# Performance work log

Hardware: AMD Instinct MI355X
Metric: run time of the kernel (lower is better)

The kernel has to match this reference:

```python
import jax, jax.numpy as jnp
import numpy as np

N, E, D, H, G, C = 50000, 800000, 3, 128, 64, 10

def setup_inputs() -> dict:
    key = jax.random.key(0)
    ks = jax.random.split(key, 10)
    s = 0.1  # small init scale
    return {
        "pos": jax.random.normal(ks[0], (N, D), jnp.float32),
        "edge_index": jax.random.randint(ks[1], (2, E), 0, N, dtype=jnp.int64),
        "batch": jnp.sort(jax.random.randint(ks[2], (N,), 0, G, dtype=jnp.int64)),
        "W1": jax.random.normal(ks[3], (D, H), jnp.float32) * s,
        "b1": jnp.zeros((H,), jnp.float32),
        "W2": jax.random.normal(ks[4], (H, H), jnp.float32) * s,
        "b2": jnp.zeros((H,), jnp.float32),
        "W3": jax.random.normal(ks[5], (H, H), jnp.float32) * s,
        "b3": jnp.zeros((H,), jnp.float32),
        "Wl1": jax.random.normal(ks[6], (H, H // 2), jnp.float32) * s,
        "bl1": jnp.zeros((H // 2,), jnp.float32),
        "Wl2": jax.random.normal(ks[7], (H // 2, C), jnp.float32) * s,
        "bl2": jnp.zeros((C,), jnp.float32),
        "num_graphs": G,
    }

def reference(pos, edge_index, batch, W1, b1, W2, b2, W3, b3, Wl1, bl1, Wl2, bl2, num_graphs):
    n = pos.shape[0]
    loop = jnp.arange(n, dtype=edge_index.dtype)
    # GCN: add self-loops, symmetric normalization deg^-1/2 (A+I) deg^-1/2
    src = jnp.concatenate([edge_index[0], loop])
    dst = jnp.concatenate([edge_index[1], loop])
    deg = jax.ops.segment_sum(jnp.ones(src.shape, pos.dtype), dst, num_segments=n)
    dinv = jax.lax.rsqrt(jnp.maximum(deg, 1e-12))  # deg >= 1 due to self-loops
    norm = dinv[src] * dinv[dst]  # [E+N]

    def gcn(x, W, b):
        h = x @ W                               # [N,F] dense transform first (PyG order)
        msg = h[src] * norm[:, None]            # gather + normalize
        return jax.ops.segment_sum(msg, dst, num_segments=n) + b  # scatter-add

    x = jax.nn.relu(gcn(pos, W1, b1))   # dropout = identity (eval mode)
    x = jax.nn.relu(gcn(x, W2, b2))
    x = jax.nn.relu(gcn(x, W3, b3))
    # global_mean_pool over batch ids
    sums = jax.ops.segment_sum(x, batch, num_segments=num_graphs)
    cnt = jax.ops.segment_sum(jnp.ones((n,), x.dtype), batch, num_segments=num_graphs)
    g = sums / jnp.maximum(cnt, 1.0)[:, None]   # [G,H]
    h = jax.nn.relu(g @ Wl1 + bl1)
    return h @ Wl2 + bl2
```

## Files before the change

kernel.cpp:

```cpp
#include <hip/hip_runtime.h>

#define H 128
#define CAP 64
#define LSTRIDE 136
#define PSTR 132
typedef unsigned int uint32;
typedef unsigned short ushort16;
typedef __attribute__((ext_vector_type(8))) short bf16x8;
typedef __attribute__((ext_vector_type(4))) float f32x4;

static __device__ __forceinline__ ushort16 f2bf(float f){
  uint32 u = __float_as_uint(f);
  uint32 r = (u + 0x7fff + ((u >> 16) & 1)) >> 16;
  return (ushort16)r;
}
static __device__ __forceinline__ float bflo(uint32 u){ return __uint_as_float(u << 16); }
static __device__ __forceinline__ float bfhi(uint32 u){ return __uint_as_float(u & 0xffff0000u); }

__global__ __launch_bounds__(256) void k_setup(int* __restrict__ deg, float* __restrict__ gsum,
                                               const int* __restrict__ batch, int n, int G,
                                               int* __restrict__ gb, int SB,
                                               const float* __restrict__ W2, const float* __restrict__ W3,
                                               ushort16* __restrict__ wp2, ushort16* __restrict__ wp3,
                                               float4* __restrict__ y0,
                                               unsigned short* __restrict__ ybA,
                                               unsigned short* __restrict__ ybB){
  int b = blockIdx.x;
  if (b < SB){
    int i = b*256 + threadIdx.x;
    if (i < n) deg[i] = 0;
    if (i < G*H) gsum[i] = 0.f;
    if (i < H){ ybA[(size_t)n*H + i] = 0; ybB[(size_t)n*H + i] = 0; }
    if (i == 0) y0[n] = make_float4(0.f, 0.f, 0.f, 0.f);
    if (i <= G){
      int lo = 0, hi = n;
      while (lo < hi){ int m = (lo + hi) >> 1; if (batch[m] < i) lo = m + 1; else hi = m; }
      gb[i] = lo;
    }
  } else {
    int gid = (b - SB)*256 + threadIdx.x;
    const float* W = (gid < 2048) ? W2 : W3;
    ushort16* wp   = (gid < 2048) ? wp2 : wp3;
    int tid = gid & 2047;
    int frag = tid >> 6, lane = tid & 63;
    int kt = frag >> 3, ct = frag & 7;
    int m = lane & 15, quad = lane >> 4;
    const float* wrow = &W[(kt*32 + quad*8)*H + ct*16 + m];
    ushort16 vals[8];
    #pragma unroll
    for (int j = 0; j < 8; j++) vals[j] = f2bf(wrow[j*H]);
    uint4 o;
    o.x = (uint32)vals[0] | ((uint32)vals[1] << 16);
    o.y = (uint32)vals[2] | ((uint32)vals[3] << 16);
    o.z = (uint32)vals[4] | ((uint32)vals[5] << 16);
    o.w = (uint32)vals[6] | ((uint32)vals[7] << 16);
    *(uint4*)&wp[(size_t)tid*8] = o;
  }
}

__global__ __launch_bounds__(256) void k_count(const int* __restrict__ dst, int E,
                                               int* __restrict__ deg, unsigned short* __restrict__ rank){
  int i = blockIdx.x*256 + threadIdx.x;
  if (i < E) rank[i] = (unsigned short)atomicAdd(&deg[dst[i]], 1);
}

__global__ __launch_bounds__(256) void k_scatter(const int* __restrict__ src, const int* __restrict__ dst,
                                                 int E, int SCB, const unsigned short* __restrict__ rank,
                                                 unsigned short* __restrict__ csr_src,
                                                 const int* __restrict__ deg, const float* __restrict__ pos,
                                                 float4* __restrict__ y0, int n){
  int b = blockIdx.x;
  if (b < SCB){
    int i = b*256 + threadIdx.x;
    if (i < E){
      int r = rank[i];
      if (r < CAP) csr_src[((size_t)dst[i] << 6) + r] = (unsigned short)src[i];
    }
  } else {
    int i = (b - SCB)*256 + threadIdx.x;
    if (i < n){
      float dv = rsqrtf((float)(deg[i] + 1));
      y0[i] = make_float4(pos[3*i]*dv, pos[3*i+1]*dv, pos[3*i+2]*dv, 0.f);
    }
  }
}

__global__ __launch_bounds__(256) void k_layer1(const float4* __restrict__ y0, const int* __restrict__ deg,
      const unsigned short* __restrict__ csr_src,
      const float* __restrict__ W1, const float* __restrict__ b1,
      ushort16* __restrict__ y1, int n){
  int node = blockIdx.x*256 + threadIdx.x;
  if (node >= n) return;
  int cnt = deg[node];
  int lo = node << 6;
  float4 own = y0[node];
  float x = own.x, y = own.y, z = own.z;
  int mm = cnt > CAP ? CAP : cnt;
  int nfull = mm >> 3, rem = mm & 7;
  #define GADD(s0,s1,s2,s3,s4,s5,s6,s7) { \
    float4 v0 = y0[s0], v1 = y0[s1], v2 = y0[s2], v3 = y0[s3]; \
    float4 v4 = y0[s4], v5 = y0[s5], v6 = y0[s6], v7 = y0[s7]; \
    x += ((v0.x+v1.x)+(v2.x+v3.x)) + ((v4.x+v5.x)+(v6.x+v7.x)); \
    y += ((v0.y+v1.y)+(v2.y+v3.y)) + ((v4.y+v5.y)+(v6.y+v7.y)); \
    z += ((v0.z+v1.z)+(v2.z+v3.z)) + ((v4.z+v5.z)+(v6.z+v7.z)); }
  if (rem){
    uint4 iv = *(const uint4*)&csr_src[lo + nfull*8];
    int s0 = (int)(iv.x & 0xffff);
    int s1 = (1 < rem)? (int)(iv.x >> 16)    : n;
    int s2 = (2 < rem)? (int)(iv.y & 0xffff) : n;
    int s3 = (3 < rem)? (int)(iv.y >> 16)    : n;
    int s4 = (4 < rem)? (int)(iv.z & 0xffff) : n;
    int s5 = (5 < rem)? (int)(iv.z >> 16)    : n;
    int s6 = (6 < rem)? (int)(iv.w & 0xffff) : n;
    int s7 = (7 < rem)? (int)(iv.w >> 16)    : n;
    GADD(s0,s1,s2,s3,s4,s5,s6,s7);
  }
  if (nfull){
    uint4 iv = *(const uint4*)&csr_src[lo];
    for (int c = 0; c < nfull; c++){
      uint4 nx = *(const uint4*)&csr_src[lo + c*8 + 8];
      int s0 = iv.x & 0xffff, s1 = iv.x >> 16;
      int s2 = iv.y & 0xffff, s3 = iv.y >> 16;
      int s4 = iv.z & 0xffff, s5 = iv.z >> 16;
      int s6 = iv.w & 0xffff, s7 = iv.w >> 16;
      GADD(s0,s1,s2,s3,s4,s5,s6,s7);
      iv = nx;
    }
  }
  #undef GADD
  float dn = rsqrtf((float)(cnt + 1));
  x *= dn; y *= dn; z *= dn;
  ushort16* rowp = &y1[(size_t)node*H];
  for (int c8 = 0; c8 < 16; c8++){
    float4 wa0 = *(const float4*)&W1[c8*8];
    float4 wa1 = *(const float4*)&W1[c8*8+4];
    float4 wb0 = *(const float4*)&W1[H + c8*8];
    float4 wb1 = *(const float4*)&W1[H + c8*8+4];
    float4 wc0 = *(const float4*)&W1[2*H + c8*8];
    float4 wc1 = *(const float4*)&W1[2*H + c8*8+4];
    float4 bb0 = *(const float4*)&b1[c8*8];
    float4 bb1 = *(const float4*)&b1[c8*8+4];
    float o0 = fmaxf(x*wa0.x + y*wb0.x + z*wc0.x + bb0.x, 0.f) * dn;
    float o1 = fmaxf(x*wa0.y + y*wb0.y + z*wc0.y + bb0.y, 0.f) * dn;
    float o2 = fmaxf(x*wa0.z + y*wb0.z + z*wc0.z + bb0.z, 0.f) * dn;
    float o3 = fmaxf(x*wa0.w + y*wb0.w + z*wc0.w + bb0.w, 0.f) * dn;
    float o4 = fmaxf(x*wa1.x + y*wb1.x + z*wc1.x + bb1.x, 0.f) * dn;
    float o5 = fmaxf(x*wa1.y + y*wb1.y + z*wc1.y + bb1.y, 0.f) * dn;
    float o6 = fmaxf(x*wa1.z + y*wb1.z + z*wc1.z + bb1.z, 0.f) * dn;
    float o7 = fmaxf(x*wa1.w + y*wb1.w + z*wc1.w + bb1.w, 0.f) * dn;
    uint4 o;
    o.x = (uint32)f2bf(o0) | ((uint32)f2bf(o1) << 16);
    o.y = (uint32)f2bf(o2) | ((uint32)f2bf(o3) << 16);
    o.z = (uint32)f2bf(o4) | ((uint32)f2bf(o5) << 16);
    o.w = (uint32)f2bf(o6) | ((uint32)f2bf(o7) << 16);
    *(uint4*)&rowp[c8*8] = o;
  }
}

template<int POOL>
__global__ __launch_bounds__(256) void k_aggdense(const ushort16* __restrict__ y, const int* __restrict__ deg,
      const unsigned short* __restrict__ csr_src, const ushort16* __restrict__ wp,
      const float* __restrict__ bias,
      ushort16* __restrict__ yout, const int* __restrict__ batch, float* __restrict__ gsum, int n){
  __shared__ unsigned short As[16*LSTRIDE];
  __shared__ float pool[POOL ? 16*PSTR : 1];
  __shared__ unsigned short outs[POOL ? 1 : 16*PSTR];
  __shared__ int sbatch[POOL ? 16 : 1];
  __shared__ float sdinv[POOL ? 1 : 16];
  int tid = threadIdx.x;
  int node16 = blockIdx.x*16;
  int nl = tid >> 4;
  int node = node16 + nl;
  int f8 = (tid & 15) * 8;

  if (tid < 16){
    int nn = node16 + tid;
    if (POOL) sbatch[tid] = (nn < n) ? batch[nn] : -1;
    else      sdinv[tid]  = (nn < n) ? rsqrtf((float)(deg[nn] + 1)) : 0.f;
  }

  float a0=0,a1=0,a2=0,a3=0,a4=0,a5=0,a6=0,a7=0;
  float dn = 0.f;
  #define ADDU(u) { a0+=bflo(u.x); a1+=bfhi(u.x); a2+=bflo(u.y); a3+=bfhi(u.y); \
                    a4+=bflo(u.z); a5+=bfhi(u.z); a6+=bflo(u.w); a7+=bfhi(u.w); }
  #define GATHER8(s0,s1,s2,s3,s4,s5,s6,s7) { \
    uint4 u0 = *(const uint4*)&y[(size_t)(s0)*H + f8]; \
    uint4 u1 = *(const uint4*)&y[(size_t)(s1)*H + f8]; \
    uint4 u2 = *(const uint4*)&y[(size_t)(s2)*H + f8]; \
    uint4 u3 = *(const uint4*)&y[(size_t)(s3)*H + f8]; \
    uint4 u4 = *(const uint4*)&y[(size_t)(s4)*H + f8]; \
    uint4 u5 = *(const uint4*)&y[(size_t)(s5)*H + f8]; \
    uint4 u6 = *(const uint4*)&y[(size_t)(s6)*H + f8]; \
    uint4 u7 = *(const uint4*)&y[(size_t)(s7)*H + f8]; \
    ADDU(u0); ADDU(u1); ADDU(u2); ADDU(u3); \
    ADDU(u4); ADDU(u5); ADDU(u6); ADDU(u7); }
  if (node < n){
    int cnt = deg[node];
    int lo = node << 6;
    dn = rsqrtf((float)(cnt + 1));
    uint4 uo = *(const uint4*)&y[(size_t)node*H + f8];
    ADDU(uo);
    int mm = cnt > CAP ? CAP : cnt;
    int nfull = mm >> 3, rem = mm & 7;
    if (rem){
      uint4 iv = *(const uint4*)&csr_src[lo + nfull*8];
      int s0 = (int)(iv.x & 0xffff);
      int s1 = (1 < rem)? (int)(iv.x >> 16)    : n;
      int s2 = (2 < rem)? (int)(iv.y & 0xffff) : n;
      int s3 = (3 < rem)? (int)(iv.y >> 16)    : n;
      int s4 = (4 < rem)? (int)(iv.z & 0xffff) : n;
      int s5 = (5 < rem)? (int)(iv.z >> 16)    : n;
      int s6 = (6 < rem)? (int)(iv.w & 0xffff) : n;
      int s7 = (7 < rem)? (int)(iv.w >> 16)    : n;
      GATHER8(s0,s1,s2,s3,s4,s5,s6,s7);
    }
    if (nfull){
      uint4 iv = *(const uint4*)&csr_src[lo];
      for (int c = 0; c < nfull; c++){
        uint4 nx = *(const uint4*)&csr_src[lo + c*8 + 8];
        int s0 = iv.x & 0xffff, s1 = iv.x >> 16;
        int s2 = iv.y & 0xffff, s3 = iv.y >> 16;
        int s4 = iv.z & 0xffff, s5 = iv.z >> 16;
        int s6 = iv.w & 0xffff, s7 = iv.w >> 16;
        GATHER8(s0,s1,s2,s3,s4,s5,s6,s7);
        iv = nx;
      }
    }
  }
  #undef GATHER8
  #undef ADDU
  uint4 o;
  o.x = (uint32)f2bf(a0*dn) | ((uint32)f2bf(a1*dn) << 16);
  o.y = (uint32)f2bf(a2*dn) | ((uint32)f2bf(a3*dn) << 16);
  o.z = (uint32)f2bf(a4*dn) | ((uint32)f2bf(a5*dn) << 16);
  o.w = (uint32)f2bf(a6*dn) | ((uint32)f2bf(a7*dn) << 16);
  *(uint4*)&As[nl*LSTRIDE + f8] = o;
  __syncthreads();

  int wave = tid >> 6;
  int lane = tid & 63;
  int m = lane & 15, quad = lane >> 4;
  f32x4 acc0 = {0.f,0.f,0.f,0.f}, acc1 = {0.f,0.f,0.f,0.f};
  int ct0 = wave*2, ct1 = wave*2 + 1;
  #pragma unroll
  for (int kt = 0; kt < 4; kt++){
    bf16x8 af = *(const bf16x8*)&As[m*LSTRIDE + kt*32 + quad*8];
    bf16x8 b0 = *(const bf16x8*)&wp[(size_t)((kt*8+ct0)*64 + lane)*8];
    bf16x8 b1 = *(const bf16x8*)&wp[(size_t)((kt*8+ct1)*64 + lane)*8];
    acc0 = __builtin_amdgcn_mfma_f32_16x16x32_bf16(af, b0, acc0, 0, 0, 0);
    acc1 = __builtin_amdgcn_mfma_f32_16x16x32_bf16(af, b1, acc1, 0, 0, 0);
  }
  #pragma unroll
  for (int j = 0; j < 2; j++){
    int ct = wave*2 + j;
    int col = ct*16 + m;
    float bv = bias[col];
    f32x4 ac = j ? acc1 : acc0;
    #pragma unroll
    for (int r = 0; r < 4; r++){
      int rl = quad*4 + r;
      int orow = node16 + rl;
      if (orow < n){
        float v = fmaxf(ac[r] + bv, 0.f);
        if (POOL) pool[rl*PSTR + col] = v;
        else      outs[rl*PSTR + col] = f2bf(v * sdinv[rl]);
      }
    }
  }
  __syncthreads();
  if (POOL){
    int col = tid & 127;
    int half = tid >> 7;
    float run = 0.f; int gprev = -1;
    for (int r = half*8; r < half*8 + 8; r++){
      int g = sbatch[r];
      if (g < 0) break;
      if (g != gprev){
        if (gprev >= 0) atomicAdd(&gsum[gprev*H + col], run);
        run = 0.f; gprev = g;
      }
      run += pool[r*PSTR + col];
    }
    if (gprev >= 0) atomicAdd(&gsum[gprev*H + col], run);
  } else {
    int row = tid >> 4;
    int orow = node16 + row;
    if (orow < n){
      const unsigned short* sp = &outs[row*PSTR + f8];
      uint4 v;
      v.x = (uint32)sp[0] | ((uint32)sp[1] << 16);
      v.y = (uint32)sp[2] | ((uint32)sp[3] << 16);
      v.z = (uint32)sp[4] | ((uint32)sp[5] << 16);
      v.w = (uint32)sp[6] | ((uint32)sp[7] << 16);
      *(uint4*)&yout[(size_t)orow*H + f8] = v;
    }
  }
}

__global__ __launch_bounds__(64) void k_head(const float* __restrict__ gsum, const int* __restrict__ gb,
            const float* __restrict__ Wl1, const float* __restrict__ bl1,
            const float* __restrict__ Wl2, const float* __restrict__ bl2,
            float* __restrict__ out){
  int g = blockIdx.x;
  int t = threadIdx.x;
  __shared__ float gs[H];
  __shared__ float h1[64];
  float inv = 1.f / fmaxf((float)(gb[g+1] - gb[g]), 1.f);
  gs[t]      = gsum[g*H + t]      * inv;
  gs[64 + t] = gsum[g*H + 64 + t] * inv;
  __syncthreads();
  float acc = bl1[t];
  for (int k = 0; k < H; k++) acc += gs[k] * Wl1[k*64 + t];
  h1[t] = fmaxf(acc, 0.f);
  __syncthreads();
  if (t < 10){
    float o = bl2[t];
    for (int j = 0; j < 64; j++) o += h1[j] * Wl2[j*10 + t];
    out[g*10 + t] = o;
  }
}

extern "C" void kernel_launch(void* const* d_in, const int* in_sizes, int n_in,
                              void* d_out, int out_size, void* d_ws, size_t ws_size,
                              hipStream_t stream){
  const float* pos = (const float*)d_in[0];
  const int*  ei   = (const int*)d_in[1];
  const int*  batch= (const int*)d_in[2];
  const float* W1 = (const float*)d_in[3];
  const float* b1 = (const float*)d_in[4];
  const float* W2 = (const float*)d_in[5];
  const float* b2 = (const float*)d_in[6];
  const float* W3 = (const float*)d_in[7];
  const float* b3 = (const float*)d_in[8];
  const float* Wl1 = (const float*)d_in[9];
  const float* bl1 = (const float*)d_in[10];
  const float* Wl2 = (const float*)d_in[11];
  const float* bl2 = (const float*)d_in[12];
  float* out = (float*)d_out;

  int N = in_sizes[0] / 3;
  int E = in_sizes[1] / 2;
  int G = out_size / 10;
  int SB = (N + 255) / 256;
  int SCB = (E + 255) / 256;
  int PB = (N + 255) / 256;

  char* p = (char*)d_ws;
  auto carve = [&](size_t bytes)->char* { char* q = p; p += (bytes + 255) & ~(size_t)255; return q; };
  int*            deg     = (int*)     carve(sizeof(int)    * (size_t)N);
  int*            gb      = (int*)     carve(sizeof(int)    * (size_t)(G+1));
  float*          gsum    = (float*)   carve(sizeof(float)  * (size_t)G * H);
  unsigned short* csr_src = (unsigned short*)carve(sizeof(unsigned short) * (size_t)(N+1) * CAP);
  unsigned short* rank    = (unsigned short*)carve(sizeof(unsigned short) * (size_t)E);
  float4*         y0      = (float4*)  carve(sizeof(float4) * (size_t)(N+1));
  ushort16*       ybufA   = (ushort16*)carve(sizeof(ushort16) * (size_t)(N+1) * H);
  ushort16*       ybufB   = (ushort16*)carve(sizeof(ushort16) * (size_t)(N+1) * H);
  ushort16*       wp2     = (ushort16*)carve(sizeof(ushort16) * 16384);
  ushort16*       wp3     = (ushort16*)carve(sizeof(ushort16) * 16384);

  const int* src = ei;
  const int* dst = ei + E;

  hipLaunchKernelGGL(k_setup, dim3(SB + 16), dim3(256), 0, stream,
                     deg, gsum, batch, N, G, gb, SB, W2, W3, wp2, wp3,
                     y0, (unsigned short*)ybufA, (unsigned short*)ybufB);

  hipLaunchKernelGGL(k_count, dim3((E+255)/256), dim3(256), 0, stream, dst, E, deg, rank);

  hipLaunchKernelGGL(k_scatter, dim3(SCB + PB), dim3(256), 0, stream,
                     src, dst, E, SCB, rank, csr_src, deg, pos, y0, N);

  hipLaunchKernelGGL(k_layer1, dim3((N+255)/256), dim3(256), 0, stream, y0, deg, csr_src, W1, b1, ybufA, N);

  hipLaunchKernelGGL(k_aggdense<0>, dim3((N+15)/16), dim3(256), 0, stream,
                     ybufA, deg, csr_src, wp2, b2, ybufB, (const int*)nullptr, (float*)nullptr, N);

  hipLaunchKernelGGL(k_aggdense<1>, dim3((N+15)/16), dim3(256), 0, stream,
                     ybufB, deg, csr_src, wp3, b3, (ushort16*)nullptr, batch, gsum, N);

  hipLaunchKernelGGL(k_head, dim3(G), dim3(64), 0, stream, gsum, gb, Wl1, bl1, Wl2, bl2, out);
}
```

Before: 230.8 us.

## Split feature buffers into column planes and separate aggregation from dense MFMA

```diff
diff --git a/kernel.cpp b/kernel.cpp
--- a/kernel.cpp
+++ b/kernel.cpp
@@ -16,6 +16,7 @@
 }
 static __device__ __forceinline__ float bflo(uint32 u){ return __uint_as_float(u << 16); }
 static __device__ __forceinline__ float bfhi(uint32 u){ return __uint_as_float(u & 0xffff0000u); }
+
 
 __global__ __launch_bounds__(256) void k_setup(int* __restrict__ deg, float* __restrict__ gsum,
                                                const int* __restrict__ batch, int n, int G,
@@ -28,9 +29,13 @@
   int b = blockIdx.x;
   if (b < SB){
     int i = b*256 + threadIdx.x;
+    size_t PL = (size_t)(n+1)*32;
     if (i < n) deg[i] = 0;
     if (i < G*H) gsum[i] = 0.f;
-    if (i < H){ ybA[(size_t)n*H + i] = 0; ybB[(size_t)n*H + i] = 0; }
+    if (i < H){
+      size_t a = (size_t)(i>>5)*PL + (size_t)n*32 + (i&31);
+      ybA[a] = 0; ybB[a] = 0;
+    }
     if (i == 0) y0[n] = make_float4(0.f, 0.f, 0.f, 0.f);
     if (i <= G){
       int lo = 0, hi = n;
@@ -88,9 +93,10 @@
 __global__ __launch_bounds__(256) void k_layer1(const float4* __restrict__ y0, const int* __restrict__ deg,
       const unsigned short* __restrict__ csr_src,
       const float* __restrict__ W1, const float* __restrict__ b1,
-      ushort16* __restrict__ y1, int n){
+      unsigned short* __restrict__ y1, int n){
   int node = blockIdx.x*256 + threadIdx.x;
   if (node >= n) return;
+  size_t PL = (size_t)(n+1)*32;
   int cnt = deg[node];
   int lo = node << 6;
   float4 own = y0[node];
@@ -130,7 +136,6 @@
   #undef GADD
   float dn = rsqrtf((float)(cnt + 1));
   x *= dn; y *= dn; z *= dn;
-  ushort16* rowp = &y1[(size_t)node*H];
   for (int c8 = 0; c8 < 16; c8++){
     float4 wa0 = *(const float4*)&W1[c8*8];
     float4 wa1 = *(const float4*)&W1[c8*8+4];
@@ -153,15 +158,81 @@
     o.y = (uint32)f2bf(o2) | ((uint32)f2bf(o3) << 16);
     o.z = (uint32)f2bf(o4) | ((uint32)f2bf(o5) << 16);
     o.w = (uint32)f2bf(o6) | ((uint32)f2bf(o7) << 16);
-    *(uint4*)&rowp[c8*8] = o;
-  }
+    *(uint4*)&y1[(size_t)(c8>>2)*PL + (size_t)node*32 + (c8&3)*8] = o;
+  }
+}
+
+__global__ __launch_bounds__(128) void k_aggcol(const unsigned short* __restrict__ y,
+      const int* __restrict__ deg, const unsigned short* __restrict__ csr_src,
+      unsigned short* __restrict__ agg, int n){
+  int b = blockIdx.x;
+  int c = b & 7;
+  int plane = c >> 1;
+  int node16 = ((b >> 3)*2 + (c & 1)) * 16;
+  int tid = threadIdx.x;
+  int nl = tid >> 3;
+  int node = node16 + nl;
+  if (node >= n) return;
+  int l4 = (tid & 7) * 4;
+  size_t PL = (size_t)(n+1)*32;
+  const unsigned short* yp = y + (size_t)plane*PL + l4;
+
+  float a0=0,a1=0,a2=0,a3=0;
+  #define ADDU2(u) { a0+=bflo(u.x); a1+=bfhi(u.x); a2+=bflo(u.y); a3+=bfhi(u.y); }
+  #define GATH8(s0,s1,s2,s3,s4,s5,s6,s7) { \
+    uint2 u0 = *(const uint2*)&yp[(size_t)(s0)*32]; \
+    uint2 u1 = *(const uint2*)&yp[(size_t)(s1)*32]; \
+    uint2 u2 = *(const uint2*)&yp[(size_t)(s2)*32]; \
+    uint2 u3 = *(const uint2*)&yp[(size_t)(s3)*32]; \
+    uint2 u4 = *(const uint2*)&yp[(size_t)(s4)*32]; \
+    uint2 u5 = *(const uint2*)&yp[(size_t)(s5)*32]; \
+    uint2 u6 = *(const uint2*)&yp[(size_t)(s6)*32]; \
+    uint2 u7 = *(const uint2*)&yp[(size_t)(s7)*32]; \
+    ADDU2(u0); ADDU2(u1); ADDU2(u2); ADDU2(u3); \
+    ADDU2(u4); ADDU2(u5); ADDU2(u6); ADDU2(u7); }
+  int cnt = deg[node];
+  int lo = node << 6;
+  uint2 uo = *(const uint2*)&yp[(size_t)node*32];
+  ADDU2(uo);
+  int mm = cnt > CAP ? CAP : cnt;
+  int nfull = mm >> 3, rem = mm & 7;
+  if (rem){
+    uint4 iv = *(const uint4*)&csr_src[lo + nfull*8];
+    int s0 = (int)(iv.x & 0xffff);
+    int s1 = (1 < rem)? (int)(iv.x >> 16)    : n;
+    int s2 = (2 < rem)? (int)(iv.y & 0xffff) : n;
+    int s3 = (3 < rem)? (int)(iv.y >> 16)    : n;
+    int s4 = (4 < rem)? (int)(iv.z & 0xffff) : n;
+    int s5 = (5 < rem)? (int)(iv.z >> 16)    : n;
+    int s6 = (6 < rem)? (int)(iv.w & 0xffff) : n;
+    int s7 = (7 < rem)? (int)(iv.w >> 16)    : n;
+    GATH8(s0,s1,s2,s3,s4,s5,s6,s7);
+  }
+  if (nfull){
+    uint4 iv = *(const uint4*)&csr_src[lo];
+    for (int cc = 0; cc < nfull; cc++){
+      uint4 nx = *(const uint4*)&csr_src[lo + cc*8 + 8];
+      int s0 = iv.x & 0xffff, s1 = iv.x >> 16;
+      int s2 = iv.y & 0xffff, s3 = iv.y >> 16;
+      int s4 = iv.z & 0xffff, s5 = iv.z >> 16;
+      int s6 = iv.w & 0xffff, s7 = iv.w >> 16;
+      GATH8(s0,s1,s2,s3,s4,s5,s6,s7);
+      iv = nx;
+    }
+  }
+  #undef GATH8
+  #undef ADDU2
+  float dn = rsqrtf((float)(cnt + 1));
+  uint2 o;
+  o.x = (uint32)f2bf(a0*dn) | ((uint32)f2bf(a1*dn) << 16);
+  o.y = (uint32)f2bf(a2*dn) | ((uint32)f2bf(a3*dn) << 16);
+  *(uint2*)&agg[(size_t)plane*PL + (size_t)node*32 + l4] = o;
 }
 
 template<int POOL>
-__global__ __launch_bounds__(256) void k_aggdense(const ushort16* __restrict__ y, const int* __restrict__ deg,
-      const unsigned short* __restrict__ csr_src, const ushort16* __restrict__ wp,
-      const float* __restrict__ bias,
-      ushort16* __restrict__ yout, const int* __restrict__ batch, float* __restrict__ gsum, int n){
+__global__ __launch_bounds__(256) void k_dense(const unsigned short* __restrict__ agg,
+      const int* __restrict__ deg, const ushort16* __restrict__ wp, const float* __restrict__ bias,
+      unsigned short* __restrict__ yout, const int* __restrict__ batch, float* __restrict__ gsum, int n){
   __shared__ unsigned short As[16*LSTRIDE];
   __shared__ float pool[POOL ? 16*PSTR : 1];
   __shared__ unsigned short outs[POOL ? 1 : 16*PSTR];
@@ -172,69 +243,16 @@
   int nl = tid >> 4;
   int node = node16 + nl;
   int f8 = (tid & 15) * 8;
+  size_t PL = (size_t)(n+1)*32;
 
   if (tid < 16){
     int nn = node16 + tid;
     if (POOL) sbatch[tid] = (nn < n) ? batch[nn] : -1;
     else      sdinv[tid]  = (nn < n) ? rsqrtf((float)(deg[nn] + 1)) : 0.f;
   }
-
-  float a0=0,a1=0,a2=0,a3=0,a4=0,a5=0,a6=0,a7=0;
-  float dn = 0.f;
-  #define ADDU(u) { a0+=bflo(u.x); a1+=bfhi(u.x); a2+=bflo(u.y); a3+=bfhi(u.y); \
-                    a4+=bflo(u.z); a5+=bfhi(u.z); a6+=bflo(u.w); a7+=bfhi(u.w); }
-  #define GATHER8(s0,s1,s2,s3,s4,s5,s6,s7) { \
-    uint4 u0 = *(const uint4*)&y[(size_t)(s0)*H + f8]; \
-    uint4 u1 = *(const uint4*)&y[(size_t)(s1)*H + f8]; \
-    uint4 u2 = *(const uint4*)&y[(size_t)(s2)*H + f8]; \
-    uint4 u3 = *(const uint4*)&y[(size_t)(s3)*H + f8]; \
-    uint4 u4 = *(const uint4*)&y[(size_t)(s4)*H + f8]; \
-    uint4 u5 = *(const uint4*)&y[(size_t)(s5)*H + f8]; \
-    uint4 u6 = *(const uint4*)&y[(size_t)(s6)*H + f8]; \
-    uint4 u7 = *(const uint4*)&y[(size_t)(s7)*H + f8]; \
-    ADDU(u0); ADDU(u1); ADDU(u2); ADDU(u3); \
-    ADDU(u4); ADDU(u5); ADDU(u6); ADDU(u7); }
-  if (node < n){
-    int cnt = deg[node];
-    int lo = node << 6;
-    dn = rsqrtf((float)(cnt + 1));
-    uint4 uo = *(const uint4*)&y[(size_t)node*H + f8];
-    ADDU(uo);
-    int mm = cnt > CAP ? CAP : cnt;
-    int nfull = mm >> 3, rem = mm & 7;
-    if (rem){
-      uint4 iv = *(const uint4*)&csr_src[lo + nfull*8];
-      int s0 = (int)(iv.x & 0xffff);
-      int s1 = (1 < rem)? (int)(iv.x >> 16)    : n;
-      int s2 = (2 < rem)? (int)(iv.y & 0xffff) : n;
-      int s3 = (3 < rem)? (int)(iv.y >> 16)    : n;
-      int s4 = (4 < rem)? (int)(iv.z & 0xffff) : n;
-      int s5 = (5 < rem)? (int)(iv.z >> 16)    : n;
-      int s6 = (6 < rem)? (int)(iv.w & 0xffff) : n;
-      int s7 = (7 < rem)? (int)(iv.w >> 16)    : n;
-      GATHER8(s0,s1,s2,s3,s4,s5,s6,s7);
-    }
-    if (nfull){
-      uint4 iv = *(const uint4*)&csr_src[lo];
-      for (int c = 0; c < nfull; c++){
-        uint4 nx = *(const uint4*)&csr_src[lo + c*8 + 8];
-        int s0 = iv.x & 0xffff, s1 = iv.x >> 16;
-        int s2 = iv.y & 0xffff, s3 = iv.y >> 16;
-        int s4 = iv.z & 0xffff, s5 = iv.z >> 16;
-        int s6 = iv.w & 0xffff, s7 = iv.w >> 16;
-        GATHER8(s0,s1,s2,s3,s4,s5,s6,s7);
-        iv = nx;
-      }
-    }
-  }
-  #undef GATHER8
-  #undef ADDU
-  uint4 o;
-  o.x = (uint32)f2bf(a0*dn) | ((uint32)f2bf(a1*dn) << 16);
-  o.y = (uint32)f2bf(a2*dn) | ((uint32)f2bf(a3*dn) << 16);
-  o.z = (uint32)f2bf(a4*dn) | ((uint32)f2bf(a5*dn) << 16);
-  o.w = (uint32)f2bf(a6*dn) | ((uint32)f2bf(a7*dn) << 16);
-  *(uint4*)&As[nl*LSTRIDE + f8] = o;
+  uint4 v = make_uint4(0,0,0,0);
+  if (node < n) v = *(const uint4*)&agg[(size_t)(f8>>5)*PL + (size_t)node*32 + (f8&31)];
+  *(uint4*)&As[nl*LSTRIDE + f8] = v;
   __syncthreads();
 
   int wave = tid >> 6;
@@ -261,9 +279,9 @@
       int rl = quad*4 + r;
       int orow = node16 + rl;
       if (orow < n){
-        float v = fmaxf(ac[r] + bv, 0.f);
-        if (POOL) pool[rl*PSTR + col] = v;
-        else      outs[rl*PSTR + col] = f2bf(v * sdinv[rl]);
+        float vv = fmaxf(ac[r] + bv, 0.f);
+        if (POOL) pool[rl*PSTR + col] = vv;
+        else      outs[rl*PSTR + col] = f2bf(vv * sdinv[rl]);
       }
     }
   }
@@ -287,12 +305,12 @@
     int orow = node16 + row;
     if (orow < n){
       const unsigned short* sp = &outs[row*PSTR + f8];
-      uint4 v;
-      v.x = (uint32)sp[0] | ((uint32)sp[1] << 16);
-      v.y = (uint32)sp[2] | ((uint32)sp[3] << 16);
-      v.z = (uint32)sp[4] | ((uint32)sp[5] << 16);
-      v.w = (uint32)sp[6] | ((uint32)sp[7] << 16);
-      *(uint4*)&yout[(size_t)orow*H + f8] = v;
+      uint4 o;
+      o.x = (uint32)sp[0] | ((uint32)sp[1] << 16);
+      o.y = (uint32)sp[2] | ((uint32)sp[3] << 16);
+      o.z = (uint32)sp[4] | ((uint32)sp[5] << 16);
+      o.w = (uint32)sp[6] | ((uint32)sp[7] << 16);
+      *(uint4*)&yout[(size_t)(f8>>5)*PL + (size_t)orow*32 + (f8&31)] = o;
     }
   }
 }
@@ -344,6 +362,7 @@
   int SB = (N + 255) / 256;
   int SCB = (E + 255) / 256;
   int PB = (N + 255) / 256;
+  int NG2 = (N + 31) / 32;
 
   char* p = (char*)d_ws;
   auto carve = [&](size_t bytes)->char* { char* q = p; p += (bytes + 255) & ~(size_t)255; return q; };
@@ -353,8 +372,9 @@
   unsigned short* csr_src = (unsigned short*)carve(sizeof(unsigned short) * (size_t)(N+1) * CAP);
   unsigned short* rank    = (unsigned short*)carve(sizeof(unsigned short) * (size_t)E);
   float4*         y0      = (float4*)  carve(sizeof(float4) * (size_t)(N+1));
-  ushort16*       ybufA   = (ushort16*)carve(sizeof(ushort16) * (size_t)(N+1) * H);
-  ushort16*       ybufB   = (ushort16*)carve(sizeof(ushort16) * (size_t)(N+1) * H);
+  unsigned short* ybufA   = (unsigned short*)carve(sizeof(unsigned short) * (size_t)(N+1) * H);
+  unsigned short* ybufB   = (unsigned short*)carve(sizeof(unsigned short) * (size_t)(N+1) * H);
+  unsigned short* aggbuf  = (unsigned short*)carve(sizeof(unsigned short) * (size_t)(N+1) * H);
   ushort16*       wp2     = (ushort16*)carve(sizeof(ushort16) * 16384);
   ushort16*       wp3     = (ushort16*)carve(sizeof(ushort16) * 16384);
 
@@ -363,7 +383,7 @@
 
   hipLaunchKernelGGL(k_setup, dim3(SB + 16), dim3(256), 0, stream,
                      deg, gsum, batch, N, G, gb, SB, W2, W3, wp2, wp3,
-                     y0, (unsigned short*)ybufA, (unsigned short*)ybufB);
+                     y0, ybufA, ybufB);
 
   hipLaunchKernelGGL(k_count, dim3((E+255)/256), dim3(256), 0, stream, dst, E, deg, rank);
 
@@ -372,11 +392,13 @@
 
   hipLaunchKernelGGL(k_layer1, dim3((N+255)/256), dim3(256), 0, stream, y0, deg, csr_src, W1, b1, ybufA, N);
 
-  hipLaunchKernelGGL(k_aggdense<0>, dim3((N+15)/16), dim3(256), 0, stream,
-                     ybufA, deg, csr_src, wp2, b2, ybufB, (const int*)nullptr, (float*)nullptr, N);
-
-  hipLaunchKernelGGL(k_aggdense<1>, dim3((N+15)/16), dim3(256), 0, stream,
-                     ybufB, deg, csr_src, wp3, b3, (ushort16*)nullptr, batch, gsum, N);
+  hipLaunchKernelGGL(k_aggcol, dim3(NG2*8), dim3(128), 0, stream, ybufA, deg, csr_src, aggbuf, N);
+  hipLaunchKernelGGL(k_dense<0>, dim3((N+15)/16), dim3(256), 0, stream,
+                     aggbuf, deg, wp2, b2, ybufB, (const int*)nullptr, (float*)nullptr, N);
+
+  hipLaunchKernelGGL(k_aggcol, dim3(NG2*8), dim3(128), 0, stream, ybufB, deg, csr_src, aggbuf, N);
+  hipLaunchKernelGGL(k_dense<1>, dim3((N+15)/16), dim3(256), 0, stream,
+                     aggbuf, deg, wp3, b3, (unsigned short*)nullptr, batch, gsum, N);
 
   hipLaunchKernelGGL(k_head, dim3(G), dim3(64), 0, stream, gsum, gb, Wl1, bl1, Wl2, bl2, out);
 }
```

New measurement: 232.1 us. Within noise of the previous version (+0.6%).
